# Kernel optimization log

Hardware: AMD Instinct MI355X
Metric: run time of the kernel (lower is better)

## Reference

```python
import jax, jax.numpy as jnp
import numpy as np

N_NODES = 50000
N_EDGES = 1600000
IN_CH, HID, OUT = 116, 256, 2


def setup_inputs() -> dict:
    key = jax.random.key(0)
    ks = jax.random.split(key, 8)
    x = jax.random.normal(ks[0], (N_NODES, IN_CH), dtype=jnp.float32)
    edge_index = jax.random.randint(ks[1], (2, N_EDGES), 0, N_NODES, dtype=jnp.int64)
    # GCNConv weights: layer l maps d_in -> d_out via x @ W + b (W stored [d_in, d_out])
    def glorot(k, di, do):
        s = jnp.sqrt(6.0 / (di + do)).astype(jnp.float32)
        return jax.random.uniform(k, (di, do), jnp.float32, -s, s)
    W1 = glorot(ks[2], IN_CH, HID); b1 = jnp.zeros((HID,), jnp.float32)
    W2 = glorot(ks[3], HID, HID);   b2 = jnp.zeros((HID,), jnp.float32)
    W3 = glorot(ks[4], HID, OUT);   b3 = jnp.zeros((OUT,), jnp.float32)
    return {"x": x, "edge_index": edge_index,
            "W1": W1, "b1": b1, "W2": W2, "b2": b2, "W3": W3, "b3": b3}


def _gcn_conv(h, W, b, src, dst, dinv):
    # PyG GCNConv (normalize=True, add_self_loops=True):
    #   out = D^{-1/2} (A + I) D^{-1/2} (h W) + b, deg counts in-edges + self loop
    hw = h @ W  # [N, d_out]
    coeff = dinv[src] * dinv[dst]                      # [E]
    msg = hw[src] * coeff[:, None]                     # [E, d_out]
    agg = jax.ops.segment_sum(msg, dst, num_segments=h.shape[0])
    agg = agg + hw * (dinv * dinv)[:, None]            # self-loop term
    return agg + b


def reference(x, edge_index, W1, b1, W2, b2, W3, b3):
    src, dst = edge_index[0], edge_index[1]
    n = x.shape[0]
    deg = jax.ops.segment_sum(jnp.ones_like(dst, dtype=x.dtype), dst, num_segments=n) + 1.0
    dinv = jax.lax.rsqrt(deg)
    h = jax.nn.relu(_gcn_conv(x, W1, b1, src, dst, dinv))
    h = jax.nn.relu(_gcn_conv(h, W2, b2, src, dst, dinv))
    out = _gcn_conv(h, W3, b3, src, dst, dinv)  # last layer: no activation (eval mode, no dropout)
    return out
```

## Files before the change

kernel.cpp:

```cpp
#include <hip/hip_runtime.h>
#include <hip/hip_bf16.h>
#include <stdint.h>

#define NN 50000
#define NE 1600000
#define INC 116
#define XBP 128
#define K1P 128
#define HID 256
#define OUTC 2

typedef float f32x4 __attribute__((ext_vector_type(4)));
typedef short s16x8 __attribute__((ext_vector_type(8)));

__device__ __forceinline__ ushort f2bf(float v) {
    uint32_t u = __float_as_uint(v);
    return (ushort)((u + 0x7FFFu + ((u >> 16) & 1u)) >> 16);
}
__device__ __forceinline__ float bf2f(ushort b) {
    return __uint_as_float(((uint32_t)b) << 16);
}
__device__ __forceinline__ float bflo(uint32_t u) { return __uint_as_float(u << 16); }
__device__ __forceinline__ float bfhi(uint32_t u) { return __uint_as_float(u & 0xFFFF0000u); }

__global__ void detect_fmt(const int* __restrict__ ebuf, int* __restrict__ flag) {
    int v = ebuf[2 * threadIdx.x + 1];
    unsigned long long b = __ballot(v != 0);
    if (threadIdx.x == 0) flag[0] = (b == 0ULL) ? 1 : 0;
}

__device__ __forceinline__ int edge_at(const int* __restrict__ ebuf, int is64, int idx) {
    return is64 ? ebuf[2 * idx] : ebuf[idx];
}

__global__ void deg_hist(const int* __restrict__ ebuf, const int* __restrict__ flag,
                         int* __restrict__ cnt) {
    int e = blockIdx.x * blockDim.x + threadIdx.x;
    if (e >= NE) return;
    int is64 = flag[0];
    int d = edge_at(ebuf, is64, NE + e);
    atomicAdd(&cnt[d], 1);
}

__global__ void dinv_kernel(const int* __restrict__ cnt, float* __restrict__ dinv) {
    int n = blockIdx.x * blockDim.x + threadIdx.x;
    if (n < NN) dinv[n] = rsqrtf((float)cnt[n] + 1.0f);
}

__global__ void scan1(const int* __restrict__ cnt, int* __restrict__ rowptr,
                      int* __restrict__ bsum) {
    __shared__ int s[256];
    int tid = threadIdx.x;
    int i = blockIdx.x * 256 + tid;
    int v = (i < NN) ? cnt[i] : 0;
    s[tid] = v;
    __syncthreads();
    for (int off = 1; off < 256; off <<= 1) {
        int t = (tid >= off) ? s[tid - off] : 0;
        __syncthreads();
        s[tid] += t;
        __syncthreads();
    }
    if (i < NN) rowptr[i] = s[tid] - v;
    if (tid == 255) bsum[blockIdx.x] = s[255];
}

__global__ void scan2(int* __restrict__ bsum, int nblocks) {
    __shared__ int s[256];
    int tid = threadIdx.x;
    int v = (tid < nblocks) ? bsum[tid] : 0;
    s[tid] = v;
    __syncthreads();
    for (int off = 1; off < 256; off <<= 1) {
        int t = (tid >= off) ? s[tid - off] : 0;
        __syncthreads();
        s[tid] += t;
        __syncthreads();
    }
    if (tid < nblocks) bsum[tid] = s[tid] - v;
}

__global__ void scan3(int* __restrict__ rowptr, const int* __restrict__ bsum,
                      int* __restrict__ fillpos) {
    int i = blockIdx.x * 256 + threadIdx.x;
    if (i < NN) {
        int r = rowptr[i] + bsum[blockIdx.x];
        rowptr[i] = r;
        fillpos[i] = r;
        if (i == NN - 1) rowptr[NN] = NE;
    }
}

__global__ void __launch_bounds__(256)
fill_csr2(const int* __restrict__ ebuf, const int* __restrict__ flag,
          int* __restrict__ fillpos, int* __restrict__ col) {
    int rng = blockIdx.x & 7;
    int lo = rng * (NN / 8), hi = lo + (NN / 8);
    int is64 = flag[0];
    int stride = (gridDim.x >> 3) * 256;
    for (int e = (blockIdx.x >> 3) * 256 + threadIdx.x; e < NE; e += stride) {
        int d = edge_at(ebuf, is64, NE + e);
        if (d >= lo && d < hi) {
            int s = edge_at(ebuf, is64, e);
            int p = atomicAdd(&fillpos[d], 1);
            col[p] = s;
        }
    }
}

__global__ void conv_x(const float* __restrict__ x, ushort* __restrict__ xb) {
    int i = blockIdx.x * 256 + threadIdx.x;
    if (i >= NN * XBP) return;
    int n = i >> 7, c = i & 127;
    xb[i] = (c < INC) ? f2bf(x[(size_t)n * INC + c]) : (ushort)0;
}

__global__ void decomp_w1(const float* __restrict__ W, ushort* __restrict__ hi,
                          ushort* __restrict__ lo) {
    int i = blockIdx.x * 256 + threadIdx.x;
    int n = i >> 7, k = i & 127;
    float v = (k < INC) ? W[k * HID + n] : 0.f;
    ushort h = f2bf(v);
    hi[n * K1P + k] = h;
    lo[n * K1P + k] = f2bf(v - bf2f(h));
}

__global__ void decomp_w2(const float* __restrict__ W, ushort* __restrict__ hi,
                          ushort* __restrict__ lo) {
    int i = blockIdx.x * 256 + threadIdx.x;
    int n = i >> 8, k = i & 255;
    float v = W[k * HID + n];
    ushort h = f2bf(v);
    hi[n * HID + k] = h;
    lo[n * HID + k] = f2bf(v - bf2f(h));
}

__global__ void __launch_bounds__(256)
agg1b(const ushort* __restrict__ xb, const float* __restrict__ x,
      const float* __restrict__ dinv, const int* __restrict__ rowptr,
      const int* __restrict__ col, ushort* __restrict__ ohi, ushort* __restrict__ olo) {
    __shared__ float red[16][16][8];
    int n = blockIdx.x, tid = threadIdx.x;
    int g = tid >> 4, c = tid & 15;
    int beg = rowptr[n], end = rowptr[n + 1];
    {
        float a0=0.f,a1=0.f,a2=0.f,a3=0.f,a4=0.f,a5=0.f,a6=0.f,a7=0.f;
        const ushort* hc = xb + c * 8;
        int j = beg + g;
        for (; j + 16 < end; j += 32) {
            int s0 = col[j], s1 = col[j + 16];
            float w0 = dinv[s0], w1 = dinv[s1];
            uint4 u0 = *(const uint4*)(hc + (size_t)s0 * XBP);
            uint4 u1 = *(const uint4*)(hc + (size_t)s1 * XBP);
            a0 += w0 * bflo(u0.x) + w1 * bflo(u1.x);
            a1 += w0 * bfhi(u0.x) + w1 * bfhi(u1.x);
            a2 += w0 * bflo(u0.y) + w1 * bflo(u1.y);
            a3 += w0 * bfhi(u0.y) + w1 * bfhi(u1.y);
            a4 += w0 * bflo(u0.z) + w1 * bflo(u1.z);
            a5 += w0 * bfhi(u0.z) + w1 * bfhi(u1.z);
            a6 += w0 * bflo(u0.w) + w1 * bflo(u1.w);
            a7 += w0 * bfhi(u0.w) + w1 * bfhi(u1.w);
        }
        if (j < end) {
            int s0 = col[j];
            float w0 = dinv[s0];
            uint4 u0 = *(const uint4*)(hc + (size_t)s0 * XBP);
            a0 += w0 * bflo(u0.x); a1 += w0 * bfhi(u0.x);
            a2 += w0 * bflo(u0.y); a3 += w0 * bfhi(u0.y);
            a4 += w0 * bflo(u0.z); a5 += w0 * bfhi(u0.z);
            a6 += w0 * bflo(u0.w); a7 += w0 * bfhi(u0.w);
        }
        red[g][c][0]=a0; red[g][c][1]=a1; red[g][c][2]=a2; red[g][c][3]=a3;
        red[g][c][4]=a4; red[g][c][5]=a5; red[g][c][6]=a6; red[g][c][7]=a7;
    }
    __syncthreads();
    int t = tid;
    if (t < K1P) {
        float s = 0.f;
        #pragma unroll
        for (int gg = 0; gg < 16; ++gg) s += red[gg][t >> 3][t & 7];
        float self = (t < INC) ? x[(size_t)n * INC + t] : 0.f;
        float dn = dinv[n];
        float r = dn * (s + dn * self);
        ushort h = f2bf(r);
        ohi[(size_t)n * K1P + t] = h;
        olo[(size_t)n * K1P + t] = f2bf(r - bf2f(h));
    }
}

__global__ void __launch_bounds__(256)
agg2b(const ushort* __restrict__ hb, const float* __restrict__ dinv,
      const int* __restrict__ rowptr, const int* __restrict__ col,
      ushort* __restrict__ ohi, ushort* __restrict__ olo) {
    __shared__ float red[8][32][8];
    int n = blockIdx.x, tid = threadIdx.x;
    int g = tid >> 5, c = tid & 31;
    int beg = rowptr[n], end = rowptr[n + 1];
    {
        float a0=0.f,a1=0.f,a2=0.f,a3=0.f,a4=0.f,a5=0.f,a6=0.f,a7=0.f;
        const ushort* hc = hb + c * 8;
        int j = beg + g;
        for (; j + 8 < end; j += 16) {
            int s0 = col[j], s1 = col[j + 8];
            float w0 = dinv[s0], w1 = dinv[s1];
            uint4 u0 = *(const uint4*)(hc + (size_t)s0 * HID);
            uint4 u1 = *(const uint4*)(hc + (size_t)s1 * HID);
            a0 += w0 * bflo(u0.x) + w1 * bflo(u1.x);
            a1 += w0 * bfhi(u0.x) + w1 * bfhi(u1.x);
            a2 += w0 * bflo(u0.y) + w1 * bflo(u1.y);
            a3 += w0 * bfhi(u0.y) + w1 * bfhi(u1.y);
            a4 += w0 * bflo(u0.z) + w1 * bflo(u1.z);
            a5 += w0 * bfhi(u0.z) + w1 * bfhi(u1.z);
            a6 += w0 * bflo(u0.w) + w1 * bflo(u1.w);
            a7 += w0 * bfhi(u0.w) + w1 * bfhi(u1.w);
        }
        if (j < end) {
            int s0 = col[j];
            float w0 = dinv[s0];
            uint4 u0 = *(const uint4*)(hc + (size_t)s0 * HID);
            a0 += w0 * bflo(u0.x); a1 += w0 * bfhi(u0.x);
            a2 += w0 * bflo(u0.y); a3 += w0 * bfhi(u0.y);
            a4 += w0 * bflo(u0.z); a5 += w0 * bfhi(u0.z);
            a6 += w0 * bflo(u0.w); a7 += w0 * bfhi(u0.w);
        }
        red[g][c][0]=a0; red[g][c][1]=a1; red[g][c][2]=a2; red[g][c][3]=a3;
        red[g][c][4]=a4; red[g][c][5]=a5; red[g][c][6]=a6; red[g][c][7]=a7;
    }
    __syncthreads();
    int t = tid;
    float s = 0.f;
    #pragma unroll
    for (int gg = 0; gg < 8; ++gg) s += red[gg][t >> 3][t & 7];
    float dn = dinv[n];
    float self = bf2f(hb[(size_t)n * HID + t]);
    float r = dn * (s + dn * self);
    ushort h = f2bf(r);
    ohi[(size_t)n * HID + t] = h;
    olo[(size_t)n * HID + t] = f2bf(r - bf2f(h));
}

template <int MODE>
__global__ void __launch_bounds__(256)
gemm_mfma(const ushort* __restrict__ Ahi, const ushort* __restrict__ Alo,
          const ushort* __restrict__ Bhi, const ushort* __restrict__ Blo,
          const float* __restrict__ bias, ushort* __restrict__ Cb,
          const float* __restrict__ W3, float* __restrict__ hw3,
          int M, int K, int Nn) {
    constexpr int BM = 128, BN = 128, BK = 32, LDK = BK + 8;
    __shared__ ushort sAh[BM * LDK], sAl[BM * LDK];
    __shared__ ushort sBh[BN * LDK], sBl[BN * LDK];
    int tid = threadIdx.x;
    int w = tid >> 6, l = tid & 63;
    int wr = w >> 1, wc = w & 1;
    int bm = blockIdx.x * BM, bn = blockIdx.y * BN;
    int l15 = l & 15, kg = l >> 4;
    f32x4 zero = {0.f, 0.f, 0.f, 0.f};
    f32x4 acc[4][4];
    #pragma unroll
    for (int i = 0; i < 4; ++i)
        #pragma unroll
        for (int j = 0; j < 4; ++j) acc[i][j] = zero;

    for (int kb = 0; kb < K; kb += BK) {
        #pragma unroll
        for (int it = 0; it < 2; ++it) {
            int cc = tid + it * 256;
            int row = cc >> 2, kp = (cc & 3) * 8;
            int ar = bm + row;
            float4 z4 = make_float4(0.f, 0.f, 0.f, 0.f);
            float4 avh = z4, avl = z4;
            if (ar < M) {
                avh = *(const float4*)(Ahi + (size_t)ar * K + kb + kp);
                avl = *(const float4*)(Alo + (size_t)ar * K + kb + kp);
            }
            *(float4*)&sAh[row * LDK + kp] = avh;
            *(float4*)&sAl[row * LDK + kp] = avl;
            int br = bn + row;
            float4 bvh = *(const float4*)(Bhi + (size_t)br * K + kb + kp);
            float4 bvl = *(const float4*)(Blo + (size_t)br * K + kb + kp);
            *(float4*)&sBh[row * LDK + kp] = bvh;
            *(float4*)&sBl[row * LDK + kp] = bvl;
        }
        __syncthreads();
        s16x8 ah[4], al[4], bh[4], bl[4];
        #pragma unroll
        for (int i = 0; i < 4; ++i) {
            int arow = wr * 64 + i * 16 + l15;
            ah[i] = *(const s16x8*)&sAh[arow * LDK + kg * 8];
            al[i] = *(const s16x8*)&sAl[arow * LDK + kg * 8];
            int brow = wc * 64 + i * 16 + l15;
            bh[i] = *(const s16x8*)&sBh[brow * LDK + kg * 8];
            bl[i] = *(const s16x8*)&sBl[brow * LDK + kg * 8];
        }
        #pragma unroll
        for (int i = 0; i < 4; ++i)
            #pragma unroll
            for (int j = 0; j < 4; ++j) {
                acc[i][j] = __builtin_amdgcn_mfma_f32_16x16x32_bf16(ah[i], bh[j], acc[i][j], 0, 0, 0);
                acc[i][j] = __builtin_amdgcn_mfma_f32_16x16x32_bf16(ah[i], bl[j], acc[i][j], 0, 0, 0);
                acc[i][j] = __builtin_amdgcn_mfma_f32_16x16x32_bf16(al[i], bh[j], acc[i][j], 0, 0, 0);
            }
        __syncthreads();
    }
    if (MODE == 1) {
        #pragma unroll
        for (int j = 0; j < 4; ++j) {
            int cn = bn + wc * 64 + j * 16 + l15;
            float bv = bias[cn];
            #pragma unroll
            for (int i = 0; i < 4; ++i) {
                int rbase = bm + wr * 64 + i * 16 + kg * 4;
                #pragma unroll
                for (int r = 0; r < 4; ++r) {
                    int rm = rbase + r;
                    if (rm < M) {
                        float v = fmaxf(acc[i][j][r] + bv, 0.f);
                        Cb[(size_t)rm * Nn + cn] = f2bf(v);
                    }
                }
            }
        }
    } else {
        float p0[4][4], p1[4][4];
        #pragma unroll
        for (int i = 0; i < 4; ++i)
            #pragma unroll
            for (int r = 0; r < 4; ++r) { p0[i][r] = 0.f; p1[i][r] = 0.f; }
        #pragma unroll
        for (int j = 0; j < 4; ++j) {
            int cn = bn + wc * 64 + j * 16 + l15;
            float bv = bias[cn];
            float w30 = W3[cn * 2 + 0], w31 = W3[cn * 2 + 1];
            #pragma unroll
            for (int i = 0; i < 4; ++i)
                #pragma unroll
                for (int r = 0; r < 4; ++r) {
                    float v = fmaxf(acc[i][j][r] + bv, 0.f);
                    p0[i][r] += v * w30;
                    p1[i][r] += v * w31;
                }
        }
        #pragma unroll
        for (int i = 0; i < 4; ++i)
            #pragma unroll
            for (int r = 0; r < 4; ++r) {
                float q0 = p0[i][r], q1 = p1[i][r];
                #pragma unroll
                for (int off = 1; off < 16; off <<= 1) {
                    q0 += __shfl_xor(q0, off);
                    q1 += __shfl_xor(q1, off);
                }
                if (l15 == 0) {
                    int rm = bm + wr * 64 + i * 16 + kg * 4 + r;
                    if (rm < M) {
                        atomicAdd(&hw3[rm * 2 + 0], q0);
                        atomicAdd(&hw3[rm * 2 + 1], q1);
                    }
                }
            }
    }
}

__global__ void agg3(const float* __restrict__ hw3, const float* __restrict__ dinv,
                     const int* __restrict__ rowptr, const int* __restrict__ col,
                     const float* __restrict__ b3, float* __restrict__ out) {
    int n = blockIdx.x * blockDim.x + threadIdx.x;
    if (n >= NN) return;
    float a0 = 0.f, a1 = 0.f;
    int beg = rowptr[n], end = rowptr[n + 1];
    for (int j = beg; j < end; ++j) {
        int s = col[j];
        float w = dinv[s];
        float2 v = ((const float2*)hw3)[s];
        a0 += w * v.x;
        a1 += w * v.y;
    }
    float dn = dinv[n];
    float2 sv = ((const float2*)hw3)[n];
    out[n * 2 + 0] = dn * (a0 + dn * sv.x) + b3[0];
    out[n * 2 + 1] = dn * (a1 + dn * sv.y) + b3[1];
}

extern "C" void kernel_launch(void* const* d_in, const int* in_sizes, int n_in,
                              void* d_out, int out_size, void* d_ws, size_t ws_size,
                              hipStream_t stream) {
    const float* x   = (const float*)d_in[0];
    const int*   ebf = (const int*)d_in[1];
    const float* W1  = (const float*)d_in[2];
    const float* b1  = (const float*)d_in[3];
    const float* W2  = (const float*)d_in[4];
    const float* b2  = (const float*)d_in[5];
    const float* W3  = (const float*)d_in[6];
    const float* b3  = (const float*)d_in[7];
    float* out = (float*)d_out;

    char* ws = (char*)d_ws;
    size_t off = 0;
    auto carve = [&](size_t bytes) -> char* {
        char* p = ws + off;
        off += (bytes + 255) & ~(size_t)255;
        return p;
    };
    int*    flag   = (int*)   carve(256);
    int*    cnt    = (int*)   carve((size_t)NN * 4);
    float*  dinv   = (float*) carve((size_t)NN * 4);
    int*    rowptr = (int*)   carve((size_t)(NN + 1) * 4);
    int*    fillpos= (int*)   carve((size_t)NN * 4);
    int*    bsum   = (int*)   carve(256 * 4);
    int*    col    = (int*)   carve((size_t)NE * 4);
    ushort* xb     = (ushort*)carve((size_t)NN * XBP * 2);
    ushort* W1thi  = (ushort*)carve((size_t)HID * K1P * 2);
    ushort* W1tlo  = (ushort*)carve((size_t)HID * K1P * 2);
    ushort* W2thi  = (ushort*)carve((size_t)HID * HID * 2);
    ushort* W2tlo  = (ushort*)carve((size_t)HID * HID * 2);
    ushort* a1hi   = (ushort*)carve((size_t)NN * K1P * 2);
    ushort* a1lo   = (ushort*)carve((size_t)NN * K1P * 2);
    ushort* h1b    = (ushort*)carve((size_t)NN * HID * 2);
    ushort* a2hi   = (ushort*)carve((size_t)NN * HID * 2);
    ushort* a2lo   = (ushort*)carve((size_t)NN * HID * 2);
    float*  hw3    = (float*) carve((size_t)NN * OUTC * 4);
    (void)ws_size; (void)n_in; (void)in_sizes; (void)out_size;

    const int SCAN_G = (NN + 255) / 256;
    const int EG     = (NE + 255) / 256;

    hipMemsetAsync(cnt, 0, (size_t)NN * 4, stream);
    hipMemsetAsync(hw3, 0, (size_t)NN * OUTC * 4, stream);
    detect_fmt<<<1, 64, 0, stream>>>(ebf, flag);
    deg_hist<<<EG, 256, 0, stream>>>(ebf, flag, cnt);
    dinv_kernel<<<SCAN_G, 256, 0, stream>>>(cnt, dinv);
    scan1<<<SCAN_G, 256, 0, stream>>>(cnt, rowptr, bsum);
    scan2<<<1, 256, 0, stream>>>(bsum, SCAN_G);
    scan3<<<SCAN_G, 256, 0, stream>>>(rowptr, bsum, fillpos);
    fill_csr2<<<2048, 256, 0, stream>>>(ebf, flag, fillpos, col);
    conv_x<<<((size_t)NN * XBP + 255) / 256, 256, 0, stream>>>(x, xb);
    decomp_w1<<<(HID * K1P) / 256, 256, 0, stream>>>(W1, W1thi, W1tlo);
    decomp_w2<<<(HID * HID) / 256, 256, 0, stream>>>(W2, W2thi, W2tlo);

    agg1b<<<NN, 256, 0, stream>>>(xb, x, dinv, rowptr, col, a1hi, a1lo);
    {
        dim3 g((NN + 127) / 128, HID / 128);
        gemm_mfma<1><<<g, 256, 0, stream>>>(a1hi, a1lo, W1thi, W1tlo, b1, h1b,
                                            nullptr, nullptr, NN, K1P, HID);
    }
    agg2b<<<NN, 256, 0, stream>>>(h1b, dinv, rowptr, col, a2hi, a2lo);
    {
        dim3 g((NN + 127) / 128, HID / 128);
        gemm_mfma<2><<<g, 256, 0, stream>>>(a2hi, a2lo, W2thi, W2tlo, b2, nullptr,
                                            W3, hw3, NN, HID, HID);
    }
    agg3<<<SCAN_G, 256, 0, stream>>>(hw3, dinv, rowptr, col, b3, out);
}
```

Baseline: 529.4 us.

## Bucket CSR neighbors by source tile and interleave aggregation node order

The degree histogram now counts each destination's edges per source bucket of 4096 nodes, and the per-(dst, bucket) offsets are used when filling the CSR. This leaves each row's neighbor list roughly sorted by source, which should give better cache locality for the gathers in the aggregation kernels. The aggregation blocks are remapped so that consecutive blocks take nodes from the eight different destination ranges, and the layer-2 gather loop is unrolled from 2 to 4 rows per iteration. In exchange it adds a 13x larger count array, an extra prefix kernel and more atomic targets.

```diff
diff --git a/kernel.cpp b/kernel.cpp
--- a/kernel.cpp
+++ b/kernel.cpp
@@ -9,6 +9,8 @@
 #define K1P 128
 #define HID 256
 #define OUTC 2
+#define NT 13
+#define TSH 12
 
 typedef float f32x4 __attribute__((ext_vector_type(4)));
 typedef short s16x8 __attribute__((ext_vector_type(8)));
@@ -33,18 +35,31 @@
     return is64 ? ebuf[2 * idx] : ebuf[idx];
 }
 
-__global__ void deg_hist(const int* __restrict__ ebuf, const int* __restrict__ flag,
-                         int* __restrict__ cnt) {
-    int e = blockIdx.x * blockDim.x + threadIdx.x;
-    if (e >= NE) return;
+__global__ void __launch_bounds__(256)
+deg_hist3(const int* __restrict__ ebuf, const int* __restrict__ flag,
+          int* __restrict__ cnt2) {
+    int rng = blockIdx.x & 7;
+    int lo = rng * (NN / 8), hi = lo + (NN / 8);
     int is64 = flag[0];
-    int d = edge_at(ebuf, is64, NE + e);
-    atomicAdd(&cnt[d], 1);
-}
-
-__global__ void dinv_kernel(const int* __restrict__ cnt, float* __restrict__ dinv) {
-    int n = blockIdx.x * blockDim.x + threadIdx.x;
-    if (n < NN) dinv[n] = rsqrtf((float)cnt[n] + 1.0f);
+    int stride = (gridDim.x >> 3) * 256;
+    for (int e = (blockIdx.x >> 3) * 256 + threadIdx.x; e < NE; e += stride) {
+        int d = edge_at(ebuf, is64, NE + e);
+        if (d >= lo && d < hi) {
+            int s = edge_at(ebuf, is64, e);
+            atomicAdd(&cnt2[d * NT + (s >> TSH)], 1);
+        }
+    }
+}
+
+__global__ void sum_cnt(const int* __restrict__ cnt2, int* __restrict__ cnt,
+                        float* __restrict__ dinv) {
+    int n = blockIdx.x * 256 + threadIdx.x;
+    if (n >= NN) return;
+    int s = 0;
+    #pragma unroll
+    for (int t = 0; t < NT; ++t) s += cnt2[n * NT + t];
+    cnt[n] = s;
+    dinv[n] = rsqrtf((float)s + 1.0f);
 }
 
 __global__ void scan1(const int* __restrict__ cnt, int* __restrict__ rowptr,
@@ -80,20 +95,29 @@
     if (tid < nblocks) bsum[tid] = s[tid] - v;
 }
 
-__global__ void scan3(int* __restrict__ rowptr, const int* __restrict__ bsum,
-                      int* __restrict__ fillpos) {
+__global__ void scan3(int* __restrict__ rowptr, const int* __restrict__ bsum) {
     int i = blockIdx.x * 256 + threadIdx.x;
     if (i < NN) {
-        int r = rowptr[i] + bsum[blockIdx.x];
-        rowptr[i] = r;
-        fillpos[i] = r;
+        rowptr[i] += bsum[blockIdx.x];
         if (i == NN - 1) rowptr[NN] = NE;
     }
 }
 
+__global__ void mk_rowptr2(const int* __restrict__ rowptr, const int* __restrict__ cnt2,
+                           int* __restrict__ fillpos2) {
+    int n = blockIdx.x * 256 + threadIdx.x;
+    if (n >= NN) return;
+    int running = rowptr[n];
+    #pragma unroll
+    for (int t = 0; t < NT; ++t) {
+        fillpos2[n * NT + t] = running;
+        running += cnt2[n * NT + t];
+    }
+}
+
 __global__ void __launch_bounds__(256)
-fill_csr2(const int* __restrict__ ebuf, const int* __restrict__ flag,
-          int* __restrict__ fillpos, int* __restrict__ col) {
+fill_csr3(const int* __restrict__ ebuf, const int* __restrict__ flag,
+          int* __restrict__ fillpos2, int* __restrict__ col) {
     int rng = blockIdx.x & 7;
     int lo = rng * (NN / 8), hi = lo + (NN / 8);
     int is64 = flag[0];
@@ -102,7 +126,7 @@
         int d = edge_at(ebuf, is64, NE + e);
         if (d >= lo && d < hi) {
             int s = edge_at(ebuf, is64, e);
-            int p = atomicAdd(&fillpos[d], 1);
+            int p = atomicAdd(&fillpos2[d * NT + (s >> TSH)], 1);
             col[p] = s;
         }
     }
@@ -140,7 +164,9 @@
       const float* __restrict__ dinv, const int* __restrict__ rowptr,
       const int* __restrict__ col, ushort* __restrict__ ohi, ushort* __restrict__ olo) {
     __shared__ float red[16][16][8];
-    int n = blockIdx.x, tid = threadIdx.x;
+    int bid = blockIdx.x;
+    int n = (bid & 7) * (NN / 8) + (bid >> 3);
+    int tid = threadIdx.x;
     int g = tid >> 4, c = tid & 15;
     int beg = rowptr[n], end = rowptr[n + 1];
     {
@@ -193,28 +219,32 @@
       const int* __restrict__ rowptr, const int* __restrict__ col,
       ushort* __restrict__ ohi, ushort* __restrict__ olo) {
     __shared__ float red[8][32][8];
-    int n = blockIdx.x, tid = threadIdx.x;
+    int bid = blockIdx.x;
+    int n = (bid & 7) * (NN / 8) + (bid >> 3);
+    int tid = threadIdx.x;
     int g = tid >> 5, c = tid & 31;
     int beg = rowptr[n], end = rowptr[n + 1];
     {
         float a0=0.f,a1=0.f,a2=0.f,a3=0.f,a4=0.f,a5=0.f,a6=0.f,a7=0.f;
         const ushort* hc = hb + c * 8;
         int j = beg + g;
-        for (; j + 8 < end; j += 16) {
-            int s0 = col[j], s1 = col[j + 8];
-            float w0 = dinv[s0], w1 = dinv[s1];
+        for (; j + 24 < end; j += 32) {
+            int s0 = col[j], s1 = col[j + 8], s2 = col[j + 16], s3 = col[j + 24];
+            float w0 = dinv[s0], w1 = dinv[s1], w2 = dinv[s2], w3 = dinv[s3];
             uint4 u0 = *(const uint4*)(hc + (size_t)s0 * HID);
             uint4 u1 = *(const uint4*)(hc + (size_t)s1 * HID);
-            a0 += w0 * bflo(u0.x) + w1 * bflo(u1.x);
-            a1 += w0 * bfhi(u0.x) + w1 * bfhi(u1.x);
-            a2 += w0 * bflo(u0.y) + w1 * bflo(u1.y);
-            a3 += w0 * bfhi(u0.y) + w1 * bfhi(u1.y);
-            a4 += w0 * bflo(u0.z) + w1 * bflo(u1.z);
-            a5 += w0 * bfhi(u0.z) + w1 * bfhi(u1.z);
-            a6 += w0 * bflo(u0.w) + w1 * bflo(u1.w);
-            a7 += w0 * bfhi(u0.w) + w1 * bfhi(u1.w);
-        }
-        if (j < end) {
+            uint4 u2 = *(const uint4*)(hc + (size_t)s2 * HID);
+            uint4 u3 = *(const uint4*)(hc + (size_t)s3 * HID);
+            a0 += w0 * bflo(u0.x) + w1 * bflo(u1.x) + w2 * bflo(u2.x) + w3 * bflo(u3.x);
+            a1 += w0 * bfhi(u0.x) + w1 * bfhi(u1.x) + w2 * bfhi(u2.x) + w3 * bfhi(u3.x);
+            a2 += w0 * bflo(u0.y) + w1 * bflo(u1.y) + w2 * bflo(u2.y) + w3 * bflo(u3.y);
+            a3 += w0 * bfhi(u0.y) + w1 * bfhi(u1.y) + w2 * bfhi(u2.y) + w3 * bfhi(u3.y);
+            a4 += w0 * bflo(u0.z) + w1 * bflo(u1.z) + w2 * bflo(u2.z) + w3 * bflo(u3.z);
+            a5 += w0 * bfhi(u0.z) + w1 * bfhi(u1.z) + w2 * bfhi(u2.z) + w3 * bfhi(u3.z);
+            a6 += w0 * bflo(u0.w) + w1 * bflo(u1.w) + w2 * bflo(u2.w) + w3 * bflo(u3.w);
+            a7 += w0 * bfhi(u0.w) + w1 * bfhi(u1.w) + w2 * bfhi(u2.w) + w3 * bfhi(u3.w);
+        }
+        for (; j < end; j += 8) {
             int s0 = col[j];
             float w0 = dinv[s0];
             uint4 u0 = *(const uint4*)(hc + (size_t)s0 * HID);
@@ -401,38 +431,39 @@
         off += (bytes + 255) & ~(size_t)255;
         return p;
     };
-    int*    flag   = (int*)   carve(256);
-    int*    cnt    = (int*)   carve((size_t)NN * 4);
-    float*  dinv   = (float*) carve((size_t)NN * 4);
-    int*    rowptr = (int*)   carve((size_t)(NN + 1) * 4);
-    int*    fillpos= (int*)   carve((size_t)NN * 4);
-    int*    bsum   = (int*)   carve(256 * 4);
-    int*    col    = (int*)   carve((size_t)NE * 4);
-    ushort* xb     = (ushort*)carve((size_t)NN * XBP * 2);
-    ushort* W1thi  = (ushort*)carve((size_t)HID * K1P * 2);
-    ushort* W1tlo  = (ushort*)carve((size_t)HID * K1P * 2);
-    ushort* W2thi  = (ushort*)carve((size_t)HID * HID * 2);
-    ushort* W2tlo  = (ushort*)carve((size_t)HID * HID * 2);
-    ushort* a1hi   = (ushort*)carve((size_t)NN * K1P * 2);
-    ushort* a1lo   = (ushort*)carve((size_t)NN * K1P * 2);
-    ushort* h1b    = (ushort*)carve((size_t)NN * HID * 2);
-    ushort* a2hi   = (ushort*)carve((size_t)NN * HID * 2);
-    ushort* a2lo   = (ushort*)carve((size_t)NN * HID * 2);
-    float*  hw3    = (float*) carve((size_t)NN * OUTC * 4);
+    int*    flag    = (int*)   carve(256);
+    int*    cnt     = (int*)   carve((size_t)NN * 4);
+    int*    cnt2    = (int*)   carve((size_t)NN * NT * 4);
+    float*  dinv    = (float*) carve((size_t)NN * 4);
+    int*    rowptr  = (int*)   carve((size_t)(NN + 1) * 4);
+    int*    fillpos2= (int*)   carve((size_t)NN * NT * 4);
+    int*    bsum    = (int*)   carve(256 * 4);
+    int*    col     = (int*)   carve((size_t)NE * 4);
+    ushort* xb      = (ushort*)carve((size_t)NN * XBP * 2);
+    ushort* W1thi   = (ushort*)carve((size_t)HID * K1P * 2);
+    ushort* W1tlo   = (ushort*)carve((size_t)HID * K1P * 2);
+    ushort* W2thi   = (ushort*)carve((size_t)HID * HID * 2);
+    ushort* W2tlo   = (ushort*)carve((size_t)HID * HID * 2);
+    ushort* a1hi    = (ushort*)carve((size_t)NN * K1P * 2);
+    ushort* a1lo    = (ushort*)carve((size_t)NN * K1P * 2);
+    ushort* h1b     = (ushort*)carve((size_t)NN * HID * 2);
+    ushort* a2hi    = (ushort*)carve((size_t)NN * HID * 2);
+    ushort* a2lo    = (ushort*)carve((size_t)NN * HID * 2);
+    float*  hw3     = (float*) carve((size_t)NN * OUTC * 4);
     (void)ws_size; (void)n_in; (void)in_sizes; (void)out_size;
 
     const int SCAN_G = (NN + 255) / 256;
-    const int EG     = (NE + 255) / 256;
-
-    hipMemsetAsync(cnt, 0, (size_t)NN * 4, stream);
+
+    hipMemsetAsync(cnt2, 0, (size_t)NN * NT * 4, stream);
     hipMemsetAsync(hw3, 0, (size_t)NN * OUTC * 4, stream);
     detect_fmt<<<1, 64, 0, stream>>>(ebf, flag);
-    deg_hist<<<EG, 256, 0, stream>>>(ebf, flag, cnt);
-    dinv_kernel<<<SCAN_G, 256, 0, stream>>>(cnt, dinv);
+    deg_hist3<<<2048, 256, 0, stream>>>(ebf, flag, cnt2);
+    sum_cnt<<<SCAN_G, 256, 0, stream>>>(cnt2, cnt, dinv);
     scan1<<<SCAN_G, 256, 0, stream>>>(cnt, rowptr, bsum);
     scan2<<<1, 256, 0, stream>>>(bsum, SCAN_G);
-    scan3<<<SCAN_G, 256, 0, stream>>>(rowptr, bsum, fillpos);
-    fill_csr2<<<2048, 256, 0, stream>>>(ebf, flag, fillpos, col);
+    scan3<<<SCAN_G, 256, 0, stream>>>(rowptr, bsum);
+    mk_rowptr2<<<SCAN_G, 256, 0, stream>>>(rowptr, cnt2, fillpos2);
+    fill_csr3<<<2048, 256, 0, stream>>>(ebf, flag, fillpos2, col);
     conv_x<<<((size_t)NN * XBP + 255) / 256, 256, 0, stream>>>(x, xb);
     decomp_w1<<<(HID * K1P) / 256, 256, 0, stream>>>(W1, W1thi, W1tlo);
     decomp_w2<<<(HID * HID) / 256, 256, 0, stream>>>(W2, W2thi, W2tlo);
```

Result: no change. 522.9 us (-1.2%).
